# Kernel tuning notes

Measured on AMD Instinct MI355X. Metric: run time of the kernel, lower is better.

## Reference

```python
import jax, jax.numpy as jnp
import numpy as np

EPS = 1e-5

def sage_layer(x, src, dst, n_tgt, Wl, bl, Wr, gamma, beta):
    # mean aggregation of source features over incoming edges per target
    msg = x[src]                                         # [E, C] irregular gather
    s = jax.ops.segment_sum(msg, dst, num_segments=n_tgt)
    cnt = jax.ops.segment_sum(jnp.ones((src.shape[0],), x.dtype), dst, num_segments=n_tgt)
    aggr = s / jnp.maximum(cnt, 1.0)[:, None]
    x_tgt = x[:n_tgt]
    h = aggr @ Wl.T + bl + x_tgt @ Wr.T                  # SAGEConv: lin_l(aggr)+lin_r(root)
    h = jax.nn.relu(h)
    mu = jnp.mean(h, axis=0)
    var = jnp.mean((h - mu) ** 2, axis=0)                # biased var (torch BN training)
    return gamma * (h - mu) * jax.lax.rsqrt(var + EPS) + beta

def setup_inputs() -> dict:
    key = jax.random.key(0)
    ks = jax.random.split(key, 16)
    C = 256
    N0, N1, N2 = 200000, 50000, 12500
    E0, E1 = 800000, 400000
    sc = 1.0 / np.sqrt(C)
    return {
        "x": jax.random.normal(ks[0], (N0, C), jnp.float32),
        "ei0_src": jax.random.randint(ks[1], (E0,), 0, N0),
        "ei0_dst": jax.random.randint(ks[2], (E0,), 0, N1),
        "ei1_src": jax.random.randint(ks[3], (E1,), 0, N1),
        "ei1_dst": jax.random.randint(ks[4], (E1,), 0, N2),
        "Wl0": jax.random.normal(ks[5], (C, C), jnp.float32) * sc,
        "bl0": jnp.zeros((C,), jnp.float32),
        "Wr0": jax.random.normal(ks[6], (C, C), jnp.float32) * sc,
        "g0": jnp.ones((C,), jnp.float32),
        "be0": jnp.zeros((C,), jnp.float32),
        "Wl1": jax.random.normal(ks[7], (C, C), jnp.float32) * sc,
        "bl1": jnp.zeros((C,), jnp.float32),
        "Wr1": jax.random.normal(ks[8], (C, C), jnp.float32) * sc,
        "g1": jnp.ones((C,), jnp.float32),
        "be1": jnp.zeros((C,), jnp.float32),
    }

def reference(x, ei0_src, ei0_dst, ei1_src, ei1_dst,
              Wl0, bl0, Wr0, g0, be0, Wl1, bl1, Wr1, g1, be1):
    N1, N2 = 50000, 12500
    x = sage_layer(x, ei0_src, ei0_dst, N1, Wl0, bl0, Wr0, g0, be0)
    x = sage_layer(x, ei1_src, ei1_dst, N2, Wl1, bl1, Wr1, g1, be1)
    return x
```

## Files before the change

kernel.cpp:

```cpp
#include <hip/hip_runtime.h>
#include <cstddef>
#include <cstdint>

#define C 256

typedef __attribute__((ext_vector_type(8))) short short8;
typedef __attribute__((ext_vector_type(4))) float f32x4;

__device__ __forceinline__ ushort f2bf(float f) {
    uint32_t u = __float_as_uint(f);
    u += 0x7FFF + ((u >> 16) & 1);
    return (ushort)(u >> 16);
}
__device__ __forceinline__ float bf2f(ushort u) {
    return __uint_as_float(((uint32_t)u) << 16);
}
__device__ __forceinline__ uint2 pack4(float a, float b, float c, float d) {
    uint2 o;
    o.x = (uint32_t)f2bf(a) | ((uint32_t)f2bf(b) << 16);
    o.y = (uint32_t)f2bf(c) | ((uint32_t)f2bf(d) << 16);
    return o;
}

__global__ void cast_kernel(const float4* __restrict__ src, uint2* __restrict__ dst, int n4) {
    int i = blockIdx.x * blockDim.x + threadIdx.x;
    if (i >= n4) return;
    float4 v = src[i];
    dst[i] = pack4(v.x, v.y, v.z, v.w);
}

__global__ void cast4_kernel(const float4* s0, const float4* s1,
                             const float4* s2, const float4* s3,
                             uint2* d0, uint2* d1, uint2* d2, uint2* d3, int n4) {
    int i = blockIdx.x * blockDim.x + threadIdx.x;
    if (i >= n4) return;
    const float4* s = (blockIdx.y == 0) ? s0 : (blockIdx.y == 1) ? s1 : (blockIdx.y == 2) ? s2 : s3;
    uint2* d = (blockIdx.y == 0) ? d0 : (blockIdx.y == 1) ? d1 : (blockIdx.y == 2) ? d2 : d3;
    float4 v = s[i];
    d[i] = pack4(v.x, v.y, v.z, v.w);
}

__global__ void hist_kernel(const int* __restrict__ dst, int* __restrict__ cnt, int E) {
    int e = blockIdx.x * blockDim.x + threadIdx.x;
    if (e < E) atomicAdd(&cnt[dst[e]], 1);
}

__global__ __launch_bounds__(1024) void scan_kernel(const int* __restrict__ cnt,
                                                    int* __restrict__ off, int n) {
    __shared__ int buf[1024];
    int chunk = (n + 1023) >> 10;
    int lo = (int)threadIdx.x * chunk;
    int hi = min(lo + chunk, n);
    int s = 0;
    for (int i = lo; i < hi; ++i) s += cnt[i];
    buf[threadIdx.x] = s;
    __syncthreads();
    int xv = s;
    for (int d = 1; d < 1024; d <<= 1) {
        int t = ((int)threadIdx.x >= d) ? buf[threadIdx.x - d] : 0;
        __syncthreads();
        xv += t;
        buf[threadIdx.x] = xv;
        __syncthreads();
    }
    int run = xv - s;
    for (int i = lo; i < hi; ++i) { off[i] = run; run += cnt[i]; }
}

__global__ void scatter_kernel(const int* __restrict__ src, const int* __restrict__ dst,
                               const int* __restrict__ off, int* __restrict__ cur,
                               int* __restrict__ esrc, int E) {
    int e = blockIdx.x * blockDim.x + threadIdx.x;
    if (e < E) {
        int d = dst[e];
        int p = off[d] + atomicAdd(&cur[d], 1);
        esrc[p] = src[e];
    }
}

__global__ __launch_bounds__(256) void aggregate_bf16_kernel(const uint2* __restrict__ xb,
        const int* __restrict__ esrc, const int* __restrict__ off,
        const int* __restrict__ cnt, uint2* __restrict__ aggr, int n_tgt) {
    int w = threadIdx.x >> 6;
    int lane = threadIdx.x & 63;
    int t = blockIdx.x * 4 + w;
    if (t >= n_tgt) return;
    int deg = cnt[t];
    int base = off[t];
    float ax = 0.f, ay = 0.f, az = 0.f, aw = 0.f;
    for (int i = 0; i < deg; ++i) {
        int s = esrc[base + i];
        uint2 v = xb[(size_t)s * 64 + lane];
        ax += bf2f((ushort)(v.x & 0xffff));
        ay += bf2f((ushort)(v.x >> 16));
        az += bf2f((ushort)(v.y & 0xffff));
        aw += bf2f((ushort)(v.y >> 16));
    }
    float inv = 1.0f / (float)(deg > 1 ? deg : 1);
    aggr[(size_t)t * 64 + lane] = pack4(ax * inv, ay * inv, az * inv, aw * inv);
}

__global__ __launch_bounds__(256) void aggregate_f32_kernel(const float4* __restrict__ x4,
        const int* __restrict__ esrc, const int* __restrict__ off,
        const int* __restrict__ cnt, uint2* __restrict__ aggr, int n_tgt) {
    int w = threadIdx.x >> 6;
    int lane = threadIdx.x & 63;
    int t = blockIdx.x * 4 + w;
    if (t >= n_tgt) return;
    int deg = cnt[t];
    int base = off[t];
    float4 acc = make_float4(0.f, 0.f, 0.f, 0.f);
    for (int i = 0; i < deg; ++i) {
        int s = esrc[base + i];
        float4 v = x4[(size_t)s * 64 + lane];
        acc.x += v.x; acc.y += v.y; acc.z += v.z; acc.w += v.w;
    }
    float inv = 1.0f / (float)(deg > 1 ? deg : 1);
    aggr[(size_t)t * 64 + lane] = pack4(acc.x * inv, acc.y * inv, acc.z * inv, acc.w * inv);
}

#define TM 128
#define TN 128
#define LDK 40

__global__ __launch_bounds__(256) void gemm_bn_mfma(
        const ushort* __restrict__ Aagg, const ushort* __restrict__ Axt,
        const ushort* __restrict__ Wl,  const ushort* __restrict__ Wr,
        const float* __restrict__ bias,
        ushort* __restrict__ h, float* __restrict__ colsum, float* __restrict__ colsq,
        int M) {
    __shared__ ushort As[TM * LDK];
    __shared__ ushort Bs[TN * LDK];
    __shared__ float csum[TN];
    __shared__ float csq[TN];

    const int tid = threadIdx.x;
    const int m0 = blockIdx.y * TM;
    const int n0 = blockIdx.x * TN;
    const int wid = tid >> 6, lane = tid & 63;
    const int l15 = lane & 15, quad = lane >> 4;
    const int wm = (wid & 1) * 64, wn = (wid >> 1) * 64;

    if (tid < TN) { csum[tid] = 0.f; csq[tid] = 0.f; }

    const int srow = tid >> 2;
    const int skoff = (tid & 3) * 8;

    f32x4 acc[4][4];
#pragma unroll
    for (int i = 0; i < 4; ++i)
#pragma unroll
        for (int j = 0; j < 4; ++j) acc[i][j] = (f32x4){0.f, 0.f, 0.f, 0.f};

#pragma unroll 1
    for (int kt = 0; kt < 16; ++kt) {
        const int ks = kt * 32;
        const ushort* Ab = (ks < 256) ? Aagg : Axt;
        const ushort* Bb = (ks < 256) ? Wl : Wr;
        const int k0 = ks & 255;
        int r0 = min(m0 + srow, M - 1);
        int r1 = min(m0 + srow + 64, M - 1);
        uint4 a0 = *(const uint4*)&Ab[(size_t)r0 * C + k0 + skoff];
        uint4 a1 = *(const uint4*)&Ab[(size_t)r1 * C + k0 + skoff];
        uint4 b0 = *(const uint4*)&Bb[(size_t)(n0 + srow) * C + k0 + skoff];
        uint4 b1 = *(const uint4*)&Bb[(size_t)(n0 + srow + 64) * C + k0 + skoff];
        __syncthreads();
        *(uint4*)&As[srow * LDK + skoff] = a0;
        *(uint4*)&As[(srow + 64) * LDK + skoff] = a1;
        *(uint4*)&Bs[srow * LDK + skoff] = b0;
        *(uint4*)&Bs[(srow + 64) * LDK + skoff] = b1;
        __syncthreads();

        short8 af[4], bw[4];
#pragma unroll
        for (int mi = 0; mi < 4; ++mi)
            af[mi] = *(const short8*)&As[(wm + mi * 16 + l15) * LDK + quad * 8];
#pragma unroll
        for (int ni = 0; ni < 4; ++ni)
            bw[ni] = *(const short8*)&Bs[(wn + ni * 16 + l15) * LDK + quad * 8];
#pragma unroll
        for (int mi = 0; mi < 4; ++mi)
#pragma unroll
            for (int ni = 0; ni < 4; ++ni)
                acc[mi][ni] = __builtin_amdgcn_mfma_f32_16x16x32_bf16(
                    af[mi], bw[ni], acc[mi][ni], 0, 0, 0);
    }

    float lsum[4] = {0.f, 0.f, 0.f, 0.f};
    float lsq[4]  = {0.f, 0.f, 0.f, 0.f};
#pragma unroll
    for (int ni = 0; ni < 4; ++ni) {
        const int col = wn + ni * 16 + l15;
        const float bv = bias[n0 + col];
#pragma unroll
        for (int mi = 0; mi < 4; ++mi) {
#pragma unroll
            for (int r = 0; r < 4; ++r) {
                int m = m0 + wm + mi * 16 + quad * 4 + r;
                float v = acc[mi][ni][r] + bv;
                v = fmaxf(v, 0.f);
                if (m < M) {
                    h[(size_t)m * C + n0 + col] = f2bf(v);
                    lsum[ni] += v;
                    lsq[ni] += v * v;
                }
            }
        }
    }
#pragma unroll
    for (int ni = 0; ni < 4; ++ni) {
        const int col = wn + ni * 16 + l15;
        atomicAdd(&csum[col], lsum[ni]);
        atomicAdd(&csq[col], lsq[ni]);
    }
    __syncthreads();
    if (tid < TN) {
        atomicAdd(&colsum[n0 + tid], csum[tid]);
        atomicAdd(&colsq[n0 + tid], csq[tid]);
    }
}

__global__ void finalize_kernel(const float* __restrict__ colsum, const float* __restrict__ colsq,
                                float* __restrict__ mu, float* __restrict__ rstd, float invN) {
    int c = threadIdx.x;
    float m = colsum[c] * invN;
    float v = colsq[c] * invN - m * m;
    mu[c] = m;
    rstd[c] = rsqrtf(fmaxf(v, 0.f) + 1e-5f);
}

__global__ void norm_bf_kernel(const uint2* __restrict__ hin,
                               const float* __restrict__ mu, const float* __restrict__ rstd,
                               const float* __restrict__ gamma, const float* __restrict__ beta,
                               uint2* __restrict__ outp, int n4) {
    int i = blockIdx.x * blockDim.x + threadIdx.x;
    if (i >= n4) return;
    int c = (i & 63) << 2;
    uint2 v = hin[i];
    float4 m = *(const float4*)&mu[c];
    float4 r = *(const float4*)&rstd[c];
    float4 g = *(const float4*)&gamma[c];
    float4 b = *(const float4*)&beta[c];
    float x0 = g.x * (bf2f((ushort)(v.x & 0xffff)) - m.x) * r.x + b.x;
    float x1 = g.y * (bf2f((ushort)(v.x >> 16))    - m.y) * r.y + b.y;
    float x2 = g.z * (bf2f((ushort)(v.y & 0xffff)) - m.z) * r.z + b.z;
    float x3 = g.w * (bf2f((ushort)(v.y >> 16))    - m.w) * r.w + b.w;
    outp[i] = pack4(x0, x1, x2, x3);
}

__global__ void norm_f32_kernel(const uint2* __restrict__ hin,
                                const float* __restrict__ mu, const float* __restrict__ rstd,
                                const float* __restrict__ gamma, const float* __restrict__ beta,
                                float4* __restrict__ outp, int n4) {
    int i = blockIdx.x * blockDim.x + threadIdx.x;
    if (i >= n4) return;
    int c = (i & 63) << 2;
    uint2 v = hin[i];
    float4 m = *(const float4*)&mu[c];
    float4 r = *(const float4*)&rstd[c];
    float4 g = *(const float4*)&gamma[c];
    float4 b = *(const float4*)&beta[c];
    float4 o;
    o.x = g.x * (bf2f((ushort)(v.x & 0xffff)) - m.x) * r.x + b.x;
    o.y = g.y * (bf2f((ushort)(v.x >> 16))    - m.y) * r.y + b.y;
    o.z = g.z * (bf2f((ushort)(v.y & 0xffff)) - m.z) * r.z + b.z;
    o.w = g.w * (bf2f((ushort)(v.y >> 16))    - m.w) * r.w + b.w;
    outp[i] = o;
}

extern "C" void kernel_launch(void* const* d_in, const int* in_sizes, int n_in,
                              void* d_out, int out_size, void* d_ws, size_t ws_size,
                              hipStream_t stream) {
    const float* x   = (const float*)d_in[0];
    const int* e0s   = (const int*)d_in[1];
    const int* e0d   = (const int*)d_in[2];
    const int* e1s   = (const int*)d_in[3];
    const int* e1d   = (const int*)d_in[4];
    const float* Wl0 = (const float*)d_in[5];
    const float* bl0 = (const float*)d_in[6];
    const float* Wr0 = (const float*)d_in[7];
    const float* ga0 = (const float*)d_in[8];
    const float* be0 = (const float*)d_in[9];
    const float* Wl1 = (const float*)d_in[10];
    const float* bl1 = (const float*)d_in[11];
    const float* Wr1 = (const float*)d_in[12];
    const float* ga1 = (const float*)d_in[13];
    const float* be1 = (const float*)d_in[14];

    const int N0 = 200000, N1 = 50000, N2 = 12500;
    const int E0 = in_sizes[1];
    const int E1 = in_sizes[3];

    char* ws = (char*)d_ws;
    size_t o = 0;
    auto alloc = [&](size_t bytes) -> char* {
        char* p = ws + o;
        o += (bytes + 255) & ~(size_t)255;
        return p;
    };

    const size_t common =
        (size_t)N1 * C * 2 * 3  + (size_t)E0 * 4 + (size_t)E1 * 4 +
        3 * (size_t)N1 * 4 + 3 * (size_t)N2 * 4 + 8 * C * 4 + 4 * (size_t)C * C * 2 + 65536;
    const bool full = ws_size >= common + (size_t)N0 * C * 2;

    ushort* x_bf  = (ushort*)alloc((full ? (size_t)N0 : (size_t)N1) * C * 2);
    ushort* aggr0 = (ushort*)alloc((size_t)N1 * C * 2);
    ushort* h0raw = (ushort*)alloc((size_t)N1 * C * 2);
    ushort* h0bf  = (ushort*)alloc((size_t)N1 * C * 2);
    ushort* aggr1 = aggr0;
    ushort* h1raw = aggr0 + (size_t)N2 * C;
    int* esrc0 = (int*)alloc((size_t)E0 * sizeof(int));
    int* esrc1 = (int*)alloc((size_t)E1 * sizeof(int));
    int* cnt0 = (int*)alloc(2 * (size_t)N1 * sizeof(int)); int* cur0 = cnt0 + N1;
    int* off0 = (int*)alloc((size_t)N1 * sizeof(int));
    int* cnt1 = (int*)alloc(2 * (size_t)N2 * sizeof(int)); int* cur1 = cnt1 + N2;
    int* off1 = (int*)alloc((size_t)N2 * sizeof(int));
    float* stats = (float*)alloc(8 * C * sizeof(float));
    float* colsum0 = stats,         *colsq0 = stats + C;
    float* mu0     = stats + 2 * C, *rstd0  = stats + 3 * C;
    float* colsum1 = stats + 4 * C, *colsq1 = stats + 5 * C;
    float* mu1     = stats + 6 * C, *rstd1  = stats + 7 * C;
    ushort* wbf = (ushort*)alloc(4 * (size_t)C * C * 2);
    ushort* wl0 = wbf, *wr0 = wbf + C * C, *wl1 = wbf + 2 * C * C, *wr1 = wbf + 3 * C * C;

    hipMemsetAsync(cnt0, 0, 2 * (size_t)N1 * sizeof(int), stream);
    hipMemsetAsync(cnt1, 0, 2 * (size_t)N2 * sizeof(int), stream);
    hipMemsetAsync(stats, 0, 8 * C * sizeof(float), stream);

    {
        int nx4 = (full ? N0 : N1) * C / 4;
        cast_kernel<<<(nx4 + 255) / 256, 256, 0, stream>>>((const float4*)x, (uint2*)x_bf, nx4);
        int nw4 = C * C / 4;
        dim3 g((nw4 + 255) / 256, 4);
        cast4_kernel<<<g, 256, 0, stream>>>((const float4*)Wl0, (const float4*)Wr0,
                                            (const float4*)Wl1, (const float4*)Wr1,
                                            (uint2*)wl0, (uint2*)wr0, (uint2*)wl1, (uint2*)wr1, nw4);
    }

    hist_kernel<<<(E0 + 255) / 256, 256, 0, stream>>>(e0d, cnt0, E0);
    scan_kernel<<<1, 1024, 0, stream>>>(cnt0, off0, N1);
    scatter_kernel<<<(E0 + 255) / 256, 256, 0, stream>>>(e0s, e0d, off0, cur0, esrc0, E0);
    if (full)
        aggregate_bf16_kernel<<<N1 / 4, 256, 0, stream>>>((const uint2*)x_bf, esrc0, off0, cnt0,
                                                          (uint2*)aggr0, N1);
    else
        aggregate_f32_kernel<<<N1 / 4, 256, 0, stream>>>((const float4*)x, esrc0, off0, cnt0,
                                                         (uint2*)aggr0, N1);
    dim3 grid0(C / TN, (N1 + TM - 1) / TM);
    gemm_bn_mfma<<<grid0, 256, 0, stream>>>(aggr0, x_bf, wl0, wr0, bl0,
                                            h0raw, colsum0, colsq0, N1);
    finalize_kernel<<<1, C, 0, stream>>>(colsum0, colsq0, mu0, rstd0, 1.0f / (float)N1);
    int n4_0 = N1 * C / 4;
    norm_bf_kernel<<<(n4_0 + 255) / 256, 256, 0, stream>>>((const uint2*)h0raw, mu0, rstd0,
                                                           ga0, be0, (uint2*)h0bf, n4_0);

    hist_kernel<<<(E1 + 255) / 256, 256, 0, stream>>>(e1d, cnt1, E1);
    scan_kernel<<<1, 1024, 0, stream>>>(cnt1, off1, N2);
    scatter_kernel<<<(E1 + 255) / 256, 256, 0, stream>>>(e1s, e1d, off1, cur1, esrc1, E1);
    aggregate_bf16_kernel<<<N2 / 4, 256, 0, stream>>>((const uint2*)h0bf, esrc1, off1, cnt1,
                                                      (uint2*)aggr1, N2);
    dim3 grid1(C / TN, (N2 + TM - 1) / TM);
    gemm_bn_mfma<<<grid1, 256, 0, stream>>>(aggr1, h0bf, wl1, wr1, bl1,
                                            h1raw, colsum1, colsq1, N2);
    finalize_kernel<<<1, C, 0, stream>>>(colsum1, colsq1, mu1, rstd1, 1.0f / (float)N2);
    int n4_1 = N2 * C / 4;
    norm_f32_kernel<<<(n4_1 + 255) / 256, 256, 0, stream>>>((const uint2*)h1raw, mu1, rstd1,
                                                            ga1, be1, (float4*)d_out, n4_1);
}
```

Before: 791.8 us.

## Fold layer-0 batchnorm into layer-1 weights and fuse preprocessing kernels

The layer-0 batchnorm affine transform is folded into the layer-1 weights and bias through a fixup kernel. This removes the layer-0 normalize pass and its extra N1xC bf16 buffer, so layer 1 aggregates the raw GEMM output directly. The cast and histogram kernels for both layers are merged into one grid-stride prep kernel, scan and scatter run for both graphs in single launches, and aggregation now uses 16-byte loads with two edges processed per wavefront. The folding leans on linearity of the mean aggregation and changes rounding, since scaled weights are cast to bf16 and pre-normalization values are aggregated.

```diff
diff --git a/kernel.cpp b/kernel.cpp
--- a/kernel.cpp
+++ b/kernel.cpp
@@ -21,32 +21,46 @@
     o.y = (uint32_t)f2bf(c) | ((uint32_t)f2bf(d) << 16);
     return o;
 }
-
-__global__ void cast_kernel(const float4* __restrict__ src, uint2* __restrict__ dst, int n4) {
+__device__ __forceinline__ void acc8(uint4 v, float* a) {
+    a[0] += bf2f((ushort)(v.x & 0xffff)); a[1] += bf2f((ushort)(v.x >> 16));
+    a[2] += bf2f((ushort)(v.y & 0xffff)); a[3] += bf2f((ushort)(v.y >> 16));
+    a[4] += bf2f((ushort)(v.z & 0xffff)); a[5] += bf2f((ushort)(v.z >> 16));
+    a[6] += bf2f((ushort)(v.w & 0xffff)); a[7] += bf2f((ushort)(v.w >> 16));
+}
+
+__global__ __launch_bounds__(256) void prep_kernel(
+        const float4* __restrict__ x, int nx4, uint2* __restrict__ xbf,
+        const float4* __restrict__ wl0f, const float4* __restrict__ wr0f,
+        uint2* __restrict__ wl0b, uint2* __restrict__ wr0b,
+        const int* __restrict__ e0d, int* __restrict__ cnt0, int E0,
+        const int* __restrict__ e1d, int* __restrict__ cnt1, int E1) {
+    const int stride = gridDim.x * blockDim.x;
     int i = blockIdx.x * blockDim.x + threadIdx.x;
-    if (i >= n4) return;
-    float4 v = src[i];
-    dst[i] = pack4(v.x, v.y, v.z, v.w);
-}
-
-__global__ void cast4_kernel(const float4* s0, const float4* s1,
-                             const float4* s2, const float4* s3,
-                             uint2* d0, uint2* d1, uint2* d2, uint2* d3, int n4) {
-    int i = blockIdx.x * blockDim.x + threadIdx.x;
-    if (i >= n4) return;
-    const float4* s = (blockIdx.y == 0) ? s0 : (blockIdx.y == 1) ? s1 : (blockIdx.y == 2) ? s2 : s3;
-    uint2* d = (blockIdx.y == 0) ? d0 : (blockIdx.y == 1) ? d1 : (blockIdx.y == 2) ? d2 : d3;
-    float4 v = s[i];
-    d[i] = pack4(v.x, v.y, v.z, v.w);
-}
-
-__global__ void hist_kernel(const int* __restrict__ dst, int* __restrict__ cnt, int E) {
-    int e = blockIdx.x * blockDim.x + threadIdx.x;
-    if (e < E) atomicAdd(&cnt[dst[e]], 1);
-}
-
-__global__ __launch_bounds__(1024) void scan_kernel(const int* __restrict__ cnt,
-                                                    int* __restrict__ off, int n) {
+    const int sec = blockIdx.y;
+    if (sec == 0) {
+        for (; i < nx4; i += stride) {
+            float4 v = x[i];
+            xbf[i] = pack4(v.x, v.y, v.z, v.w);
+        }
+    } else if (sec == 1) {
+        const int nw4 = C * C / 4;
+        for (; i < 2 * nw4; i += stride) {
+            if (i < nw4) { float4 v = wl0f[i]; wl0b[i] = pack4(v.x, v.y, v.z, v.w); }
+            else { float4 v = wr0f[i - nw4]; wr0b[i - nw4] = pack4(v.x, v.y, v.z, v.w); }
+        }
+    } else if (sec == 2) {
+        for (; i < E0; i += stride) atomicAdd(&cnt0[e0d[i]], 1);
+    } else {
+        for (; i < E1; i += stride) atomicAdd(&cnt1[e1d[i]], 1);
+    }
+}
+
+__global__ __launch_bounds__(1024) void scan2_kernel(
+        const int* __restrict__ cnt0, int* __restrict__ off0, int n0,
+        const int* __restrict__ cnt1, int* __restrict__ off1, int n1) {
+    const int* cnt = blockIdx.x ? cnt1 : cnt0;
+    int* off = blockIdx.x ? off1 : off0;
+    int n = blockIdx.x ? n1 : n0;
     __shared__ int buf[1024];
     int chunk = (n + 1023) >> 10;
     int lo = (int)threadIdx.x * chunk;
@@ -67,37 +81,54 @@
     for (int i = lo; i < hi; ++i) { off[i] = run; run += cnt[i]; }
 }
 
-__global__ void scatter_kernel(const int* __restrict__ src, const int* __restrict__ dst,
-                               const int* __restrict__ off, int* __restrict__ cur,
-                               int* __restrict__ esrc, int E) {
+__global__ void scatter2_kernel(
+        const int* __restrict__ s0, const int* __restrict__ d0,
+        const int* __restrict__ off0, int* __restrict__ cur0, int* __restrict__ esrc0, int E0,
+        const int* __restrict__ s1, const int* __restrict__ d1,
+        const int* __restrict__ off1, int* __restrict__ cur1, int* __restrict__ esrc1, int E1) {
     int e = blockIdx.x * blockDim.x + threadIdx.x;
-    if (e < E) {
-        int d = dst[e];
-        int p = off[d] + atomicAdd(&cur[d], 1);
-        esrc[p] = src[e];
-    }
-}
-
-__global__ __launch_bounds__(256) void aggregate_bf16_kernel(const uint2* __restrict__ xb,
+    if (e < E0) {
+        int d = d0[e];
+        esrc0[off0[d] + atomicAdd(&cur0[d], 1)] = s0[e];
+    } else if (e < E0 + E1) {
+        int i = e - E0;
+        int d = d1[i];
+        esrc1[off1[d] + atomicAdd(&cur1[d], 1)] = s1[i];
+    }
+}
+
+__global__ __launch_bounds__(256) void aggregate_kernel(const uint4* __restrict__ xb4,
         const int* __restrict__ esrc, const int* __restrict__ off,
-        const int* __restrict__ cnt, uint2* __restrict__ aggr, int n_tgt) {
-    int w = threadIdx.x >> 6;
-    int lane = threadIdx.x & 63;
-    int t = blockIdx.x * 4 + w;
+        const int* __restrict__ cnt, uint4* __restrict__ out4, int n_tgt) {
+    const int lane = threadIdx.x & 63;
+    const int half = lane >> 5, l31 = lane & 31;
+    const int t = blockIdx.x * 4 + (threadIdx.x >> 6);
     if (t >= n_tgt) return;
-    int deg = cnt[t];
-    int base = off[t];
-    float ax = 0.f, ay = 0.f, az = 0.f, aw = 0.f;
-    for (int i = 0; i < deg; ++i) {
-        int s = esrc[base + i];
-        uint2 v = xb[(size_t)s * 64 + lane];
-        ax += bf2f((ushort)(v.x & 0xffff));
-        ay += bf2f((ushort)(v.x >> 16));
-        az += bf2f((ushort)(v.y & 0xffff));
-        aw += bf2f((ushort)(v.y >> 16));
-    }
-    float inv = 1.0f / (float)(deg > 1 ? deg : 1);
-    aggr[(size_t)t * 64 + lane] = pack4(ax * inv, ay * inv, az * inv, aw * inv);
+    const int deg = cnt[t];
+    const int base = off[t];
+    float a[8] = {0.f, 0.f, 0.f, 0.f, 0.f, 0.f, 0.f, 0.f};
+    const int deg2 = deg & ~1;
+    for (int i = 0; i < deg2; i += 2) {
+        int s = esrc[base + i + half];
+        uint4 v = xb4[(size_t)s * 32 + l31];
+        acc8(v, a);
+    }
+    if ((deg & 1) && half == 0) {
+        int s = esrc[base + deg - 1];
+        uint4 v = xb4[(size_t)s * 32 + l31];
+        acc8(v, a);
+    }
+#pragma unroll
+    for (int j = 0; j < 8; ++j) a[j] += __shfl_xor(a[j], 32, 64);
+    if (half == 0) {
+        float inv = 1.0f / (float)(deg > 1 ? deg : 1);
+        uint4 o;
+        o.x = (uint32_t)f2bf(a[0] * inv) | ((uint32_t)f2bf(a[1] * inv) << 16);
+        o.y = (uint32_t)f2bf(a[2] * inv) | ((uint32_t)f2bf(a[3] * inv) << 16);
+        o.z = (uint32_t)f2bf(a[4] * inv) | ((uint32_t)f2bf(a[5] * inv) << 16);
+        o.w = (uint32_t)f2bf(a[6] * inv) | ((uint32_t)f2bf(a[7] * inv) << 16);
+        out4[(size_t)t * 32 + l31] = o;
+    }
 }
 
 __global__ __launch_bounds__(256) void aggregate_f32_kernel(const float4* __restrict__ x4,
@@ -220,51 +251,60 @@
     }
 }
 
-__global__ void finalize_kernel(const float* __restrict__ colsum, const float* __restrict__ colsq,
-                                float* __restrict__ mu, float* __restrict__ rstd, float invN) {
-    int c = threadIdx.x;
-    float m = colsum[c] * invN;
-    float v = colsq[c] * invN - m * m;
-    mu[c] = m;
-    rstd[c] = rsqrtf(fmaxf(v, 0.f) + 1e-5f);
-}
-
-__global__ void norm_bf_kernel(const uint2* __restrict__ hin,
-                               const float* __restrict__ mu, const float* __restrict__ rstd,
-                               const float* __restrict__ gamma, const float* __restrict__ beta,
-                               uint2* __restrict__ outp, int n4) {
+__global__ __launch_bounds__(256) void fixup_kernel(
+        const float* __restrict__ colsum, const float* __restrict__ colsq, float invN,
+        const float* __restrict__ g0, const float* __restrict__ be0,
+        const float* __restrict__ Wl1, const float* __restrict__ Wr1,
+        const float* __restrict__ bl1,
+        ushort* __restrict__ wl1b, ushort* __restrict__ wr1b, float* __restrict__ bias1) {
+    __shared__ float ss[C], st[C];
+    __shared__ float red[256];
+    const int k = threadIdx.x;
+    {
+        float m = colsum[k] * invN;
+        float v = colsq[k] * invN - m * m;
+        float r = rsqrtf(fmaxf(v, 0.f) + 1e-5f);
+        float s = g0[k] * r;
+        ss[k] = s;
+        st[k] = be0[k] - m * s;
+    }
+    __syncthreads();
+    const int n = blockIdx.x;
+    float wl = Wl1[(size_t)n * C + k];
+    float wr = Wr1[(size_t)n * C + k];
+    wl1b[(size_t)n * C + k] = f2bf(wl * ss[k]);
+    wr1b[(size_t)n * C + k] = f2bf(wr * ss[k]);
+    red[k] = st[k] * (wl + wr);
+    __syncthreads();
+    for (int d = 128; d > 0; d >>= 1) {
+        if (k < d) red[k] += red[k + d];
+        __syncthreads();
+    }
+    if (k == 0) bias1[n] = bl1[n] + red[0];
+}
+
+__global__ __launch_bounds__(256) void norm1_kernel(const uint2* __restrict__ hin,
+        const float* __restrict__ colsum, const float* __restrict__ colsq, float invN,
+        const float* __restrict__ gamma, const float* __restrict__ beta,
+        float4* __restrict__ outp, int n4) {
+    __shared__ float smu[C], srs[C];
+    {
+        int k = threadIdx.x;
+        float m = colsum[k] * invN;
+        float v = colsq[k] * invN - m * m;
+        smu[k] = m;
+        srs[k] = rsqrtf(fmaxf(v, 0.f) + 1e-5f);
+    }
+    __syncthreads();
     int i = blockIdx.x * blockDim.x + threadIdx.x;
     if (i >= n4) return;
     int c = (i & 63) << 2;
     uint2 v = hin[i];
-    float4 m = *(const float4*)&mu[c];
-    float4 r = *(const float4*)&rstd[c];
-    float4 g = *(const float4*)&gamma[c];
-    float4 b = *(const float4*)&beta[c];
-    float x0 = g.x * (bf2f((ushort)(v.x & 0xffff)) - m.x) * r.x + b.x;
-    float x1 = g.y * (bf2f((ushort)(v.x >> 16))    - m.y) * r.y + b.y;
-    float x2 = g.z * (bf2f((ushort)(v.y & 0xffff)) - m.z) * r.z + b.z;
-    float x3 = g.w * (bf2f((ushort)(v.y >> 16))    - m.w) * r.w + b.w;
-    outp[i] = pack4(x0, x1, x2, x3);
-}
-
-__global__ void norm_f32_kernel(const uint2* __restrict__ hin,
-                                const float* __restrict__ mu, const float* __restrict__ rstd,
-                                const float* __restrict__ gamma, const float* __restrict__ beta,
-                                float4* __restrict__ outp, int n4) {
-    int i = blockIdx.x * blockDim.x + threadIdx.x;
-    if (i >= n4) return;
-    int c = (i & 63) << 2;
-    uint2 v = hin[i];
-    float4 m = *(const float4*)&mu[c];
-    float4 r = *(const float4*)&rstd[c];
-    float4 g = *(const float4*)&gamma[c];
-    float4 b = *(const float4*)&beta[c];
     float4 o;
-    o.x = g.x * (bf2f((ushort)(v.x & 0xffff)) - m.x) * r.x + b.x;
-    o.y = g.y * (bf2f((ushort)(v.x >> 16))    - m.y) * r.y + b.y;
-    o.z = g.z * (bf2f((ushort)(v.y & 0xffff)) - m.z) * r.z + b.z;
-    o.w = g.w * (bf2f((ushort)(v.y >> 16))    - m.w) * r.w + b.w;
+    o.x = gamma[c + 0] * (bf2f((ushort)(v.x & 0xffff)) - smu[c + 0]) * srs[c + 0] + beta[c + 0];
+    o.y = gamma[c + 1] * (bf2f((ushort)(v.x >> 16))    - smu[c + 1]) * srs[c + 1] + beta[c + 1];
+    o.z = gamma[c + 2] * (bf2f((ushort)(v.y & 0xffff)) - smu[c + 2]) * srs[c + 2] + beta[c + 2];
+    o.w = gamma[c + 3] * (bf2f((ushort)(v.y >> 16))    - smu[c + 3]) * srs[c + 3] + beta[c + 3];
     outp[i] = o;
 }
 
@@ -300,14 +340,14 @@
     };
 
     const size_t common =
-        (size_t)N1 * C * 2 * 3  + (size_t)E0 * 4 + (size_t)E1 * 4 +
-        3 * (size_t)N1 * 4 + 3 * (size_t)N2 * 4 + 8 * C * 4 + 4 * (size_t)C * C * 2 + 65536;
+        (size_t)N1 * C * 2 * 2  + (size_t)E0 * 4 + (size_t)E1 * 4 +
+        3 * (size_t)N1 * 4 + 3 * (size_t)N2 * 4 + 8 * C * 4 + 4 * (size_t)C * C * 2 +
+        C * 4 + 65536;
     const bool full = ws_size >= common + (size_t)N0 * C * 2;
 
     ushort* x_bf  = (ushort*)alloc((full ? (size_t)N0 : (size_t)N1) * C * 2);
     ushort* aggr0 = (ushort*)alloc((size_t)N1 * C * 2);
     ushort* h0raw = (ushort*)alloc((size_t)N1 * C * 2);
-    ushort* h0bf  = (ushort*)alloc((size_t)N1 * C * 2);
     ushort* aggr1 = aggr0;
     ushort* h1raw = aggr0 + (size_t)N2 * C;
     int* esrc0 = (int*)alloc((size_t)E0 * sizeof(int));
@@ -318,11 +358,10 @@
     int* off1 = (int*)alloc((size_t)N2 * sizeof(int));
     float* stats = (float*)alloc(8 * C * sizeof(float));
     float* colsum0 = stats,         *colsq0 = stats + C;
-    float* mu0     = stats + 2 * C, *rstd0  = stats + 3 * C;
     float* colsum1 = stats + 4 * C, *colsq1 = stats + 5 * C;
-    float* mu1     = stats + 6 * C, *rstd1  = stats + 7 * C;
     ushort* wbf = (ushort*)alloc(4 * (size_t)C * C * 2);
-    ushort* wl0 = wbf, *wr0 = wbf + C * C, *wl1 = wbf + 2 * C * C, *wr1 = wbf + 3 * C * C;
+    ushort* wl0b = wbf, *wr0b = wbf + C * C, *wl1b = wbf + 2 * C * C, *wr1b = wbf + 3 * C * C;
+    float* bias1 = (float*)alloc(C * sizeof(float));
 
     hipMemsetAsync(cnt0, 0, 2 * (size_t)N1 * sizeof(int), stream);
     hipMemsetAsync(cnt1, 0, 2 * (size_t)N2 * sizeof(int), stream);
@@ -330,41 +369,35 @@
 
     {
         int nx4 = (full ? N0 : N1) * C / 4;
-        cast_kernel<<<(nx4 + 255) / 256, 256, 0, stream>>>((const float4*)x, (uint2*)x_bf, nx4);
-        int nw4 = C * C / 4;
-        dim3 g((nw4 + 255) / 256, 4);
-        cast4_kernel<<<g, 256, 0, stream>>>((const float4*)Wl0, (const float4*)Wr0,
-                                            (const float4*)Wl1, (const float4*)Wr1,
-                                            (uint2*)wl0, (uint2*)wr0, (uint2*)wl1, (uint2*)wr1, nw4);
-    }
-
-    hist_kernel<<<(E0 + 255) / 256, 256, 0, stream>>>(e0d, cnt0, E0);
-    scan_kernel<<<1, 1024, 0, stream>>>(cnt0, off0, N1);
-    scatter_kernel<<<(E0 + 255) / 256, 256, 0, stream>>>(e0s, e0d, off0, cur0, esrc0, E0);
+        dim3 g(2048, 4);
+        prep_kernel<<<g, 256, 0, stream>>>((const float4*)x, nx4, (uint2*)x_bf,
+                                           (const float4*)Wl0, (const float4*)Wr0,
+                                           (uint2*)wl0b, (uint2*)wr0b,
+                                           e0d, cnt0, E0, e1d, cnt1, E1);
+    }
+    scan2_kernel<<<2, 1024, 0, stream>>>(cnt0, off0, N1, cnt1, off1, N2);
+    scatter2_kernel<<<(E0 + E1 + 255) / 256, 256, 0, stream>>>(
+        e0s, e0d, off0, cur0, esrc0, E0, e1s, e1d, off1, cur1, esrc1, E1);
+
     if (full)
-        aggregate_bf16_kernel<<<N1 / 4, 256, 0, stream>>>((const uint2*)x_bf, esrc0, off0, cnt0,
-                                                          (uint2*)aggr0, N1);
+        aggregate_kernel<<<N1 / 4, 256, 0, stream>>>((const uint4*)x_bf, esrc0, off0, cnt0,
+                                                     (uint4*)aggr0, N1);
     else
         aggregate_f32_kernel<<<N1 / 4, 256, 0, stream>>>((const float4*)x, esrc0, off0, cnt0,
                                                          (uint2*)aggr0, N1);
     dim3 grid0(C / TN, (N1 + TM - 1) / TM);
-    gemm_bn_mfma<<<grid0, 256, 0, stream>>>(aggr0, x_bf, wl0, wr0, bl0,
+    gemm_bn_mfma<<<grid0, 256, 0, stream>>>(aggr0, x_bf, wl0b, wr0b, bl0,
                                             h0raw, colsum0, colsq0, N1);
-    finalize_kernel<<<1, C, 0, stream>>>(colsum0, colsq0, mu0, rstd0, 1.0f / (float)N1);
-    int n4_0 = N1 * C / 4;
-    norm_bf_kernel<<<(n4_0 + 255) / 256, 256, 0, stream>>>((const uint2*)h0raw, mu0, rstd0,
-                                                           ga0, be0, (uint2*)h0bf, n4_0);
-
-    hist_kernel<<<(E1 + 255) / 256, 256, 0, stream>>>(e1d, cnt1, E1);
-    scan_kernel<<<1, 1024, 0, stream>>>(cnt1, off1, N2);
-    scatter_kernel<<<(E1 + 255) / 256, 256, 0, stream>>>(e1s, e1d, off1, cur1, esrc1, E1);
-    aggregate_bf16_kernel<<<N2 / 4, 256, 0, stream>>>((const uint2*)h0bf, esrc1, off1, cnt1,
-                                                      (uint2*)aggr1, N2);
+    fixup_kernel<<<C, 256, 0, stream>>>(colsum0, colsq0, 1.0f / (float)N1,
+                                        ga0, be0, Wl1, Wr1, bl1, wl1b, wr1b, bias1);
+
+    aggregate_kernel<<<N2 / 4, 256, 0, stream>>>((const uint4*)h0raw, esrc1, off1, cnt1,
+                                                 (uint4*)aggr1, N2);
     dim3 grid1(C / TN, (N2 + TM - 1) / TM);
-    gemm_bn_mfma<<<grid1, 256, 0, stream>>>(aggr1, h0bf, wl1, wr1, bl1,
+    gemm_bn_mfma<<<grid1, 256, 0, stream>>>(aggr1, h0raw, wl1b, wr1b, bias1,
                                             h1raw, colsum1, colsq1, N2);
-    finalize_kernel<<<1, C, 0, stream>>>(colsum1, colsq1, mu1, rstd1, 1.0f / (float)N2);
     int n4_1 = N2 * C / 4;
-    norm_f32_kernel<<<(n4_1 + 255) / 256, 256, 0, stream>>>((const uint2*)h1raw, mu1, rstd1,
-                                                            ga1, be1, (float4*)d_out, n4_1);
-}
+    norm1_kernel<<<(n4_1 + 255) / 256, 256, 0, stream>>>((const uint2*)h1raw,
+                                                         colsum1, colsq1, 1.0f / (float)N2,
+                                                         ga1, be1, (float4*)d_out, n4_1);
+}
```

Result: faster. 707.6 us (-10.6%).
